# Performance work log

Measured on AMD Instinct MI355X. Metric: run time of the kernel, lower is better.

The kernel has to match this reference:

```python
import jax, jax.numpy as jnp
import numpy as np

N_ELEC = 8192   # electrons (nodes)
N_NUC = 512     # nuclei
EMB = 256       # embedding_dim
KER = 256       # kernel_dim
DF = 64         # dist_feat_dim
MID = 128       # round(sqrt(DF*KER)), log-interpolated hidden width of w-MLP
E = 131072      # edges per edge type


def _ssp(x):
    # shifted softplus, deepqmc default activation: log(0.5*exp(x) + 0.5)
    return jax.nn.softplus(x) - jnp.log(2.0)


def setup_inputs() -> dict:
    key = jax.random.key(0)
    ks = jax.random.split(key, 24)
    def nrm(k, shape, scale):
        return jax.random.normal(k, shape, dtype=jnp.float32) * scale
    inp = {}
    inp['electrons'] = nrm(ks[0], (N_ELEC, EMB), 1.0)
    inp['nuclei'] = nrm(ks[1], (N_NUC, KER), 1.0)
    for i, lbl in enumerate(['same', 'anti', 'n']):
        inp[f'dist_{lbl}'] = jax.random.uniform(ks[2 + i], (E, DF), dtype=jnp.float32)
        inp[f'w1_{lbl}'] = nrm(ks[5 + i], (DF, MID), DF ** -0.5)
        inp[f'b1_{lbl}'] = jnp.zeros((MID,), jnp.float32)
        inp[f'w2_{lbl}'] = nrm(ks[8 + i], (MID, KER), MID ** -0.5)
        inp[f'g_{lbl}'] = nrm(ks[11 + i], (KER, EMB), KER ** -0.5)
    inp['h_w'] = nrm(ks[14], (EMB, KER), EMB ** -0.5)
    inp['senders_same'] = jax.random.randint(ks[15], (E,), 0, N_ELEC)
    inp['senders_anti'] = jax.random.randint(ks[16], (E,), 0, N_ELEC)
    inp['senders_n'] = jax.random.randint(ks[17], (E,), 0, N_NUC)
    inp['receivers_same'] = jax.random.randint(ks[18], (E,), 0, N_ELEC)
    inp['receivers_anti'] = jax.random.randint(ks[19], (E,), 0, N_ELEC)
    inp['receivers_n'] = jax.random.randint(ks[20], (E,), 0, N_ELEC)
    return inp


def reference(electrons, nuclei, dist_same, dist_anti, dist_n,
              w1_same, b1_same, w2_same, w1_anti, b1_anti, w2_anti,
              w1_n, b1_n, w2_n, g_same, g_anti, g_n, h_w,
              senders_same, senders_anti, senders_n,
              receivers_same, receivers_anti, receivers_n):
    def w_mlp(d, w1, b1, w2):
        # MLP with ('log', 2) hidden layers: linear+bias -> SSP -> last linear (no bias)
        return _ssp(d @ w1 + b1) @ w2

    # per-edge filters from distance features: [E, KER]
    we_same = w_mlp(dist_same, w1_same, b1_same, w2_same)
    we_anti = w_mlp(dist_anti, w1_anti, b1_anti, w2_anti)
    we_n = w_mlp(dist_n, w1_n, b1_n, w2_n)

    # shared h (single bias-free linear) on gathered sender electrons: [E, KER]
    hx_same = electrons[senders_same] @ h_w
    hx_anti = electrons[senders_anti] @ h_w

    weh_same = we_same * hx_same
    weh_anti = we_anti * hx_anti
    weh_n = we_n * nuclei[senders_n]

    # scatter-sum messages to receiver electrons: [N_ELEC, KER]
    z_same = jax.ops.segment_sum(weh_same, receivers_same, num_segments=N_ELEC)
    z_anti = jax.ops.segment_sum(weh_anti, receivers_anti, num_segments=N_ELEC)
    z_n = jax.ops.segment_sum(weh_n, receivers_n, num_segments=N_ELEC)

    # per-label g (single bias-free linear) + residual update, order matches original
    return electrons + (z_n @ g_n + z_same @ g_same + z_anti @ g_anti)
```

## Files before the change

kernel.cpp:

```cpp
#include <hip/hip_runtime.h>
#include <stdint.h>


#define N_ELEC 8192
#define N_NUC  512
#define EMB    256
#define KER    256
#define DF     64
#define MID    128
#define NEDGE  131072
#define RPS    8256
#define CSTR   272
#define ASTR_HE 528
#define ASTR_FN 1552

using u16 = unsigned short;
using u64 = unsigned long long;
typedef short short8 __attribute__((ext_vector_type(8)));
typedef float f32x4 __attribute__((ext_vector_type(4)));

__device__ __forceinline__ float bf2f(u16 h) {
  return __uint_as_float(((unsigned)h) << 16);
}
__device__ __forceinline__ u16 f2bf(float f) {
  unsigned u = __float_as_uint(f);
  return (u16)((u + 0x7FFFu + ((u >> 16) & 1u)) >> 16);
}
__device__ __forceinline__ unsigned pkbf(float a, float b) {
  return ((unsigned)f2bf(b) << 16) | (unsigned)f2bf(a);
}
__device__ __forceinline__ float ssp_fast(float x) {
  const float e = __expf(-fabsf(x));
  return fmaxf(x, 0.f) + __logf(fmaf(0.5f, e, 0.5f));
}

__device__ __forceinline__ void bar_lds() {
  __builtin_amdgcn_sched_barrier(0);
  asm volatile("s_waitcnt lgkmcnt(0)" ::: "memory");
  __builtin_amdgcn_s_barrier();
  __builtin_amdgcn_sched_barrier(0);
}

__global__ __launch_bounds__(256) void k_setup(
    const float* h_w, const float* w1s, const float* w1a, const float* w1n,
    const float* w2s, const float* w2a, const float* w2n, const float* gs,
    const float* ga, const float* gn, const int* r0, const int* r1,
    const int* r2, u16* hwT, u16* w1T, u16* w2T, u16* gT, float4* z,
    int* cnt) {
  const int b = blockIdx.x;
  if (b < 6144) {
    z[b * 256 + threadIdx.x] = (float4){0.f, 0.f, 0.f, 0.f};
    return;
  }
  if (b >= 7648) {
    const int eb = b - 7648;
    const int t = eb >> 9;
    const int* rcv = t == 0 ? r0 : (t == 1 ? r1 : r2);
    const int e = ((eb & 511) << 8) + threadIdx.x;
    atomicAdd(&cnt[t * N_ELEC + rcv[e]], 1);
    return;
  }
  int i = (b - 6144) * 256 + threadIdx.x;
  if (i < 65536) {
    int n = i >> 8, k = i & 255;
    hwT[i] = f2bf(h_w[k * 256 + n]);
    return;
  }
  int j = i - 65536;
  if (j < 24576) {
    int t = j >> 13, jj = j & 8191, n = jj >> 6, k = jj & 63;
    const float* w1 = t == 0 ? w1s : (t == 1 ? w1a : w1n);
    w1T[j] = f2bf(w1[k * 128 + n]);
    return;
  }
  j -= 24576;
  if (j < 98304) {
    int t = j >> 15, jj = j & 32767, n = jj >> 7, k = jj & 127;
    const float* w2 = t == 0 ? w2s : (t == 1 ? w2a : w2n);
    w2T[j] = f2bf(w2[k * 256 + n]);
    return;
  }
  j -= 98304;
  if (j < 196608) {
    int n = j / 768, q = j % 768, t = q >> 8, k = q & 255;
    const float* g = t == 0 ? gs : (t == 1 ? ga : gn);
    gT[j] = f2bf(g[k * 256 + n]);
  }
}

__global__ __launch_bounds__(256) void k_scan(const int* cnt, int* rowptr,
                                              int* cursor) {
  const int t = blockIdx.x, tid = threadIdx.x;
  __shared__ int part[256];
  const int* c = cnt + t * N_ELEC;
  int s = 0;
#pragma unroll
  for (int i = 0; i < 32; ++i) s += c[tid * 32 + i];
  part[tid] = s;
  __syncthreads();
  for (int off = 1; off < 256; off <<= 1) {
    int v = (tid >= off) ? part[tid - off] : 0;
    __syncthreads();
    part[tid] += v;
    __syncthreads();
  }
  int run = (tid == 0) ? 0 : part[tid - 1];
  int* rp = rowptr + t * RPS;
  int* cu = cursor + t * N_ELEC;
  for (int i = 0; i < 32; ++i) {
    rp[tid * 32 + i] = run;
    cu[tid * 32 + i] = run;
    run += c[tid * 32 + i];
  }
  if (tid == 255) rp[N_ELEC] = run;
}

__global__ __launch_bounds__(256) void k_place_he(
    const int* r0, const int* r1, const int* r2, const int* s0, const int* s1,
    const int* s2, int* cursor, u64* pk, const float* elec, const u16* hwT,
    u16* he) {
  __shared__ __align__(16) char As[32 * ASTR_HE];
  const int bid = blockIdx.x, tid = threadIdx.x;
  if (bid < 1536) {
    const int t = bid >> 9;
    const int* rcv = t == 0 ? r0 : (t == 1 ? r1 : r2);
    const int* snd = t == 0 ? s0 : (t == 1 ? s1 : s2);
    const int e = ((bid & 511) << 8) + tid;
    const int rr = rcv[e];
    const int pos = atomicAdd(&cursor[t * N_ELEC + rr], 1);
    pk[t * NEDGE + pos] = (u64)(unsigned)e | ((u64)(unsigned)snd[e] << 17) |
                          ((u64)(unsigned)rr << 30);
    return;
  }
  const int m0 = (bid - 1536) * 32;
#pragma unroll
  for (int i = 0; i < 16; ++i) {
    const int idx = i * 256 + tid;
    const int row = idx >> 7, cp = idx & 127;
    const float2 v = *(const float2*)(elec + (long)(m0 + row) * 256 + cp * 2);
    *(unsigned*)(As + row * ASTR_HE + cp * 4) = pkbf(v.x, v.y);
  }
  __syncthreads();
  const int l = tid & 63, lane15 = l & 15, quad = l >> 4, wv = tid >> 6;
  const int nw = wv * 64;
  f32x4 acc[2][4];
#pragma unroll
  for (int i = 0; i < 2; ++i)
#pragma unroll
    for (int j = 0; j < 4; ++j) acc[i][j] = (f32x4){0.f, 0.f, 0.f, 0.f};
  for (int kt = 0; kt < 256; kt += 32) {
    short8 af[2], bf[4];
#pragma unroll
    for (int i = 0; i < 2; ++i)
      af[i] = *(const short8*)(As + (i * 16 + lane15) * ASTR_HE + kt * 2 +
                               quad * 16);
#pragma unroll
    for (int i = 0; i < 4; ++i)
      bf[i] = *(const short8*)(hwT + (nw + i * 16 + lane15) * 256 + kt +
                               quad * 8);
#pragma unroll
    for (int mi = 0; mi < 2; ++mi)
#pragma unroll
      for (int ni = 0; ni < 4; ++ni)
        acc[mi][ni] = __builtin_amdgcn_mfma_f32_16x16x32_bf16(
            af[mi], bf[ni], acc[mi][ni], 0, 0, 0);
  }
#pragma unroll
  for (int mi = 0; mi < 2; ++mi)
#pragma unroll
    for (int r = 0; r < 4; ++r) {
      const int row = m0 + mi * 16 + quad * 4 + r;
#pragma unroll
      for (int ni = 0; ni < 4; ++ni) {
        const int col = nw + ni * 16 + lane15;
        he[row * 256 + col] = f2bf(acc[mi][ni][r]);
      }
    }
}

__global__ __launch_bounds__(256, 3) void k_edge(
    const float* d0, const float* d1, const float* d2, const float* b0,
    const float* b1p, const float* b2, const u16* w1T, const u16* w2T,
    const u16* he, const float* nucf, const u64* pk, float* z) {
  __shared__ char mid[128 * CSTR];
  __shared__ char hc[64 * CSTR];
  __shared__ int snd_l[128], rcv_l[128];

  const int t = blockIdx.z;
  const int m0 = blockIdx.x * 128;
  const int tid = threadIdx.x;
  const float* dist = t == 0 ? d0 : (t == 1 ? d1 : d2);
  const float* bias = t == 0 ? b0 : (t == 1 ? b1p : b2);
  const u16* w1t = w1T + t * 8192;
  const u16* w2t = w2T + t * 32768;
  const bool is_nuc = (t == 2);
  const u64* pkt = pk + (size_t)t * NEDGE + m0;

  if (tid < 128) {
    const u64 rec = pkt[tid];
    snd_l[tid] = (int)((rec >> 17) & 0x1FFFu);
    rcv_l[tid] = (int)(rec >> 30);
  }

  int rows[4];
#pragma unroll
  for (int s = 0; s < 4; ++s)
    rows[s] = (int)(pkt[(s * 256 + tid) >> 3] & 0x1FFFFu);
#pragma unroll
  for (int j = 0; j < 2; ++j)
#pragma unroll
    for (int s = 0; s < 4; ++s) {
      const int idx = s * 256 + tid, row = idx >> 3, ch = idx & 7;
      const float4 v =
          *(const float4*)(dist + (long)rows[s] * 64 + j * 32 + ch * 4);
      uint2 p;
      p.x = pkbf(v.x, v.y);
      p.y = pkbf(v.z, v.w);
      *(uint2*)(mid + j * 8192 + row * 64 + ch * 8) = p;
    }
  bar_lds();

  const int l = tid & 63, lane15 = l & 15, quad = l >> 4, wv = tid >> 6;
  const int mw = (wv >> 1) * 64, nw = (wv & 1) * 64;

  f32x4 acc[4][4];
#pragma unroll
  for (int i = 0; i < 4; ++i)
#pragma unroll
    for (int j = 0; j < 4; ++j) acc[i][j] = (f32x4){0.f, 0.f, 0.f, 0.f};
#pragma unroll
  for (int j = 0; j < 2; ++j) {
    short8 af[4], bf[4];
#pragma unroll
    for (int i = 0; i < 4; ++i) {
      af[i] = *(const short8*)(mid + j * 8192 + (mw + i * 16 + lane15) * 64 +
                               quad * 16);
      bf[i] = *(const short8*)(w1t + (nw + i * 16 + lane15) * 64 + j * 32 +
                               quad * 8);
    }
    __builtin_amdgcn_s_setprio(1);
#pragma unroll
    for (int mi = 0; mi < 4; ++mi)
#pragma unroll
      for (int ni = 0; ni < 4; ++ni)
        acc[mi][ni] = __builtin_amdgcn_mfma_f32_16x16x32_bf16(
            af[mi], bf[ni], acc[mi][ni], 0, 0, 0);
    __builtin_amdgcn_s_setprio(0);
  }
  bar_lds();

#pragma unroll
  for (int mi = 0; mi < 4; ++mi)
#pragma unroll
    for (int r = 0; r < 4; ++r) {
      const int row = mw + mi * 16 + quad * 4 + r;
#pragma unroll
      for (int ni = 0; ni < 4; ++ni) {
        const int col = nw + ni * 16 + lane15;
        const float x = acc[mi][ni][r] + bias[col];
        *(u16*)(mid + row * CSTR + col * 2) = f2bf(ssp_fast(x));
      }
    }
  bar_lds();

  for (int n0 = 0; n0 < 256; n0 += 128) {
#pragma unroll
    for (int i = 0; i < 4; ++i)
#pragma unroll
      for (int j = 0; j < 4; ++j) acc[i][j] = (f32x4){0.f, 0.f, 0.f, 0.f};
#pragma unroll
    for (int kt = 0; kt < 128; kt += 32) {
      short8 af[4], bf[4];
#pragma unroll
      for (int i = 0; i < 4; ++i) {
        af[i] = *(const short8*)(mid + (mw + i * 16 + lane15) * CSTR + kt * 2 +
                                 quad * 16);
        bf[i] = *(const short8*)(w2t + (n0 + nw + i * 16 + lane15) * 128 + kt +
                                 quad * 8);
      }
      __builtin_amdgcn_s_setprio(1);
#pragma unroll
      for (int mi = 0; mi < 4; ++mi)
#pragma unroll
        for (int ni = 0; ni < 4; ++ni)
          acc[mi][ni] = __builtin_amdgcn_mfma_f32_16x16x32_bf16(
              af[mi], bf[ni], acc[mi][ni], 0, 0, 0);
      __builtin_amdgcn_s_setprio(0);
    }

    for (int h = 0; h < 2; ++h) {
      const int rbase = h * 64;
      if (!is_nuc) {
#pragma unroll
        for (int c = 0; c < 4; ++c) {
          const int chunk = c * 256 + tid;
          const int row = chunk >> 4, off = chunk & 15;
          const uint4 v =
              *(const uint4*)((const char*)he +
                              (size_t)snd_l[rbase + row] * 512 + n0 * 2 +
                              off * 16);
          *(uint4*)(hc + row * CSTR + off * 16) = v;
        }
      } else {
#pragma unroll
        for (int c = 0; c < 4; ++c) {
          const int chunk = c * 256 + tid;
          const int row = chunk >> 4, off = chunk & 15;
          const char* src = (const char*)nucf +
                            (size_t)snd_l[rbase + row] * 1024 + n0 * 4 +
                            off * 32;
          const float4 a = *(const float4*)src;
          const float4 b = *(const float4*)(src + 16);
          uint4 p;
          p.x = pkbf(a.x, a.y);
          p.y = pkbf(a.z, a.w);
          p.z = pkbf(b.x, b.y);
          p.w = pkbf(b.z, b.w);
          *(uint4*)(hc + row * CSTR + off * 16) = p;
        }
      }
      bar_lds();

      if ((wv >> 1) == h) {
#pragma unroll
        for (int mi = 0; mi < 4; ++mi)
#pragma unroll
          for (int r = 0; r < 4; ++r) {
            const int lrow = mi * 16 + quad * 4 + r;
#pragma unroll
            for (int ni = 0; ni < 4; ++ni) {
              const int col = nw + ni * 16 + lane15;
              u16* p = (u16*)(hc + lrow * CSTR) + col;
              *p = f2bf(acc[mi][ni][r] * bf2f(*p));
            }
          }
      }
      bar_lds();

      {
        const int cp = l;
        const int rbeg = wv * 16, rend = rbeg + 16;
        float a0 = 0.f, a1 = 0.f;
        int cur = rcv_l[rbase + rbeg];
        for (int row = rbeg; row < rend; ++row) {
          const unsigned p = *(const unsigned*)(hc + row * CSTR + cp * 4);
          a0 += __uint_as_float(p << 16);
          a1 += __uint_as_float(p & 0xffff0000u);
          const int nxt = (row + 1 < rend) ? rcv_l[rbase + row + 1] : -1;
          if (nxt != cur) {
            float* zp = z + (size_t)cur * 768 + t * 256 + n0 + cp * 2;
            unsafeAtomicAdd(zp, a0);
            unsafeAtomicAdd(zp + 1, a1);
            a0 = a1 = 0.f;
            cur = nxt;
          }
        }
      }
      bar_lds();
    }
  }
}

__global__ __launch_bounds__(256) void k_final(const float* z, const u16* gT,
                                               const float* elec, float* out) {
  __shared__ __align__(16) char As[32 * ASTR_FN];
  const int tid = threadIdx.x;
  const int m0 = blockIdx.x * 32;
#pragma unroll
  for (int i = 0; i < 24; ++i) {
    const int idx = i * 256 + tid;
    const int row = idx / 192, q = idx % 192;
    const float4 v = *(const float4*)(z + (long)(m0 + row) * 768 + q * 4);
    uint2 p;
    p.x = pkbf(v.x, v.y);
    p.y = pkbf(v.z, v.w);
    *(uint2*)(As + row * ASTR_FN + q * 8) = p;
  }
  __syncthreads();
  const int l = tid & 63, lane15 = l & 15, quad = l >> 4, wv = tid >> 6;
  const int nw = wv * 64;
  f32x4 acc[2][4];
#pragma unroll
  for (int i = 0; i < 2; ++i)
#pragma unroll
    for (int j = 0; j < 4; ++j) acc[i][j] = (f32x4){0.f, 0.f, 0.f, 0.f};
  for (int kt = 0; kt < 768; kt += 32) {
    short8 af[2], bf[4];
#pragma unroll
    for (int i = 0; i < 2; ++i)
      af[i] = *(const short8*)(As + (i * 16 + lane15) * ASTR_FN + kt * 2 +
                               quad * 16);
#pragma unroll
    for (int i = 0; i < 4; ++i)
      bf[i] = *(const short8*)(gT + (nw + i * 16 + lane15) * 768 + kt +
                               quad * 8);
#pragma unroll
    for (int mi = 0; mi < 2; ++mi)
#pragma unroll
      for (int ni = 0; ni < 4; ++ni)
        acc[mi][ni] = __builtin_amdgcn_mfma_f32_16x16x32_bf16(
            af[mi], bf[ni], acc[mi][ni], 0, 0, 0);
  }
#pragma unroll
  for (int mi = 0; mi < 2; ++mi)
#pragma unroll
    for (int r = 0; r < 4; ++r) {
      const int row = m0 + mi * 16 + quad * 4 + r;
#pragma unroll
      for (int ni = 0; ni < 4; ++ni) {
        const int col = nw + ni * 16 + lane15;
        out[row * 256 + col] = acc[mi][ni][r] + elec[row * 256 + col];
      }
    }
}

extern "C" void kernel_launch(void* const* d_in, const int* in_sizes, int n_in,
                              void* d_out, int out_size, void* d_ws,
                              size_t ws_size, hipStream_t stream) {
  int I_dist[3], I_w1[3], I_b1[3], I_w2[3], I_g[3], I_hw;
  if (in_sizes[3] == 64 * 128) {
    for (int t = 0; t < 3; ++t) {
      I_dist[t] = 2 + t * 5 + 0;
      I_w1[t] = 2 + t * 5 + 1;
      I_b1[t] = 2 + t * 5 + 2;
      I_w2[t] = 2 + t * 5 + 3;
      I_g[t] = 2 + t * 5 + 4;
    }
    I_hw = 17;
  } else {
    I_dist[0] = 2; I_dist[1] = 3; I_dist[2] = 4;
    I_w1[0] = 5;  I_b1[0] = 6;  I_w2[0] = 7;
    I_w1[1] = 8;  I_b1[1] = 9;  I_w2[1] = 10;
    I_w1[2] = 11; I_b1[2] = 12; I_w2[2] = 13;
    I_g[0] = 14; I_g[1] = 15; I_g[2] = 16;
    I_hw = 17;
  }
  const int I_snd[3] = {18, 19, 20};
  const int I_rcv[3] = {21, 22, 23};

  char* ws = (char*)d_ws;
  u16* he = (u16*)(ws + 0);
  u16* hwT = (u16*)(ws + 4194304);
  u16* w1T = (u16*)(ws + 4325376);
  u16* w2T = (u16*)(ws + 4374528);
  u16* gT = (u16*)(ws + 4571136);
  float* z = (float*)(ws + 4964352);
  int* cnt = (int*)(ws + 30130176);
  int* rowptr = (int*)(ws + 30228480);
  int* cursor = (int*)(ws + 30327552);
  u64* pk = (u64*)(ws + 30425856);

  const float* elec = (const float*)d_in[0];
  const float* nuc = (const float*)d_in[1];
  const int* s0 = (const int*)d_in[I_snd[0]];
  const int* s1 = (const int*)d_in[I_snd[1]];
  const int* s2 = (const int*)d_in[I_snd[2]];
  const int* r0 = (const int*)d_in[I_rcv[0]];
  const int* r1 = (const int*)d_in[I_rcv[1]];
  const int* r2 = (const int*)d_in[I_rcv[2]];

  hipMemsetAsync(cnt, 0, 98304, stream);

  k_setup<<<9184, 256, 0, stream>>>(
      (const float*)d_in[I_hw], (const float*)d_in[I_w1[0]],
      (const float*)d_in[I_w1[1]], (const float*)d_in[I_w1[2]],
      (const float*)d_in[I_w2[0]], (const float*)d_in[I_w2[1]],
      (const float*)d_in[I_w2[2]], (const float*)d_in[I_g[0]],
      (const float*)d_in[I_g[1]], (const float*)d_in[I_g[2]], r0, r1, r2,
      hwT, w1T, w2T, gT, (float4*)z, cnt);

  k_scan<<<3, 256, 0, stream>>>(cnt, rowptr, cursor);

  k_place_he<<<1792, 256, 0, stream>>>(r0, r1, r2, s0, s1, s2, cursor, pk,
                                       elec, hwT, he);

  k_edge<<<dim3(NEDGE / 128, 1, 3), 256, 0, stream>>>(
      (const float*)d_in[I_dist[0]], (const float*)d_in[I_dist[1]],
      (const float*)d_in[I_dist[2]], (const float*)d_in[I_b1[0]],
      (const float*)d_in[I_b1[1]], (const float*)d_in[I_b1[2]], w1T, w2T, he,
      nuc, pk, z);

  k_final<<<N_ELEC / 32, 256, 0, stream>>>(z, gT, elec, (float*)d_out);
}
```

Measured before the change: 391.6 us.

## Make edge kernel persistent with prefetch of next tile's indices and distances

The edge kernel now launches 256 blocks per edge type, and each block loops over 4 tiles of 128 edges with a stride of 256 tiles. While the first MLP layer of the current tile runs, it prefetches the next tile's packed sender/receiver records and its distance features into registers, hiding the gather latency behind MFMA work. The risk is higher register pressure from holding eight float4 prefetch buffers, which could reduce occupancy below the 3 blocks per CU target. It also cuts the grid from 3072 to 768 blocks, which may leave some CUs underused or unevenly loaded.

Result: slower. 475.9 us (+21.5%).

```diff
diff --git a/kernel.cpp b/kernel.cpp
--- a/kernel.cpp
+++ b/kernel.cpp
@@ -187,95 +187,78 @@
   __shared__ int snd_l[128], rcv_l[128];
 
   const int t = blockIdx.z;
-  const int m0 = blockIdx.x * 128;
   const int tid = threadIdx.x;
   const float* dist = t == 0 ? d0 : (t == 1 ? d1 : d2);
   const float* bias = t == 0 ? b0 : (t == 1 ? b1p : b2);
   const u16* w1t = w1T + t * 8192;
   const u16* w2t = w2T + t * 32768;
   const bool is_nuc = (t == 2);
-  const u64* pkt = pk + (size_t)t * NEDGE + m0;
-
-  if (tid < 128) {
-    const u64 rec = pkt[tid];
-    snd_l[tid] = (int)((rec >> 17) & 0x1FFFu);
-    rcv_l[tid] = (int)(rec >> 30);
-  }
-
-  int rows[4];
-#pragma unroll
-  for (int s = 0; s < 4; ++s)
-    rows[s] = (int)(pkt[(s * 256 + tid) >> 3] & 0x1FFFFu);
-#pragma unroll
-  for (int j = 0; j < 2; ++j)
-#pragma unroll
-    for (int s = 0; s < 4; ++s) {
-      const int idx = s * 256 + tid, row = idx >> 3, ch = idx & 7;
-      const float4 v =
-          *(const float4*)(dist + (long)rows[s] * 64 + j * 32 + ch * 4);
-      uint2 p;
-      p.x = pkbf(v.x, v.y);
-      p.y = pkbf(v.z, v.w);
-      *(uint2*)(mid + j * 8192 + row * 64 + ch * 8) = p;
-    }
-  bar_lds();
+  const u64* pkbase = pk + (size_t)t * NEDGE;
 
   const int l = tid & 63, lane15 = l & 15, quad = l >> 4, wv = tid >> 6;
   const int mw = (wv >> 1) * 64, nw = (wv & 1) * 64;
 
-  f32x4 acc[4][4];
-#pragma unroll
-  for (int i = 0; i < 4; ++i)
-#pragma unroll
-    for (int j = 0; j < 4; ++j) acc[i][j] = (f32x4){0.f, 0.f, 0.f, 0.f};
-#pragma unroll
-  for (int j = 0; j < 2; ++j) {
-    short8 af[4], bf[4];
-#pragma unroll
-    for (int i = 0; i < 4; ++i) {
-      af[i] = *(const short8*)(mid + j * 8192 + (mw + i * 16 + lane15) * 64 +
-                               quad * 16);
-      bf[i] = *(const short8*)(w1t + (nw + i * 16 + lane15) * 64 + j * 32 +
-                               quad * 8);
-    }
-    __builtin_amdgcn_s_setprio(1);
-#pragma unroll
-    for (int mi = 0; mi < 4; ++mi)
-#pragma unroll
-      for (int ni = 0; ni < 4; ++ni)
-        acc[mi][ni] = __builtin_amdgcn_mfma_f32_16x16x32_bf16(
-            af[mi], bf[ni], acc[mi][ni], 0, 0, 0);
-    __builtin_amdgcn_s_setprio(0);
-  }
-  bar_lds();
-
-#pragma unroll
-  for (int mi = 0; mi < 4; ++mi)
-#pragma unroll
-    for (int r = 0; r < 4; ++r) {
-      const int row = mw + mi * 16 + quad * 4 + r;
-#pragma unroll
-      for (int ni = 0; ni < 4; ++ni) {
-        const int col = nw + ni * 16 + lane15;
-        const float x = acc[mi][ni][r] + bias[col];
-        *(u16*)(mid + row * CSTR + col * 2) = f2bf(ssp_fast(x));
-      }
-    }
-  bar_lds();
-
-  for (int n0 = 0; n0 < 256; n0 += 128) {
+  int tile = blockIdx.x;
+  u64 rec_pf = 0;
+  int rows_pf[4];
+  float4 dv[2][4];
+  {
+    const u64* pkt = pkbase + (size_t)tile * 128;
+    if (tid < 128) rec_pf = pkt[tid];
+#pragma unroll
+    for (int s = 0; s < 4; ++s)
+      rows_pf[s] = (int)(pkt[(s * 256 + tid) >> 3] & 0x1FFFFu);
+#pragma unroll
+    for (int j = 0; j < 2; ++j)
+#pragma unroll
+      for (int s = 0; s < 4; ++s) {
+        const int ch = (s * 256 + tid) & 7;
+        dv[j][s] =
+            *(const float4*)(dist + (long)rows_pf[s] * 64 + j * 32 + ch * 4);
+      }
+  }
+
+  for (int it = 0; it < 4; ++it) {
+    if (tid < 128) {
+      snd_l[tid] = (int)((rec_pf >> 17) & 0x1FFFu);
+      rcv_l[tid] = (int)(rec_pf >> 30);
+    }
+#pragma unroll
+    for (int j = 0; j < 2; ++j)
+#pragma unroll
+      for (int s = 0; s < 4; ++s) {
+        const int idx = s * 256 + tid, row = idx >> 3, ch = idx & 7;
+        uint2 p;
+        p.x = pkbf(dv[j][s].x, dv[j][s].y);
+        p.y = pkbf(dv[j][s].z, dv[j][s].w);
+        *(uint2*)(mid + j * 8192 + row * 64 + ch * 8) = p;
+      }
+    bar_lds();
+
+    u64 rec_n = 0;
+    int rows_n[4];
+    const int ntile = tile + 256;
+    if (it < 3) {
+      const u64* pn = pkbase + (size_t)ntile * 128;
+      if (tid < 128) rec_n = pn[tid];
+#pragma unroll
+      for (int s = 0; s < 4; ++s)
+        rows_n[s] = (int)(pn[(s * 256 + tid) >> 3] & 0x1FFFFu);
+    }
+
+    f32x4 acc[4][4];
 #pragma unroll
     for (int i = 0; i < 4; ++i)
 #pragma unroll
       for (int j = 0; j < 4; ++j) acc[i][j] = (f32x4){0.f, 0.f, 0.f, 0.f};
 #pragma unroll
-    for (int kt = 0; kt < 128; kt += 32) {
+    for (int j = 0; j < 2; ++j) {
       short8 af[4], bf[4];
 #pragma unroll
       for (int i = 0; i < 4; ++i) {
-        af[i] = *(const short8*)(mid + (mw + i * 16 + lane15) * CSTR + kt * 2 +
+        af[i] = *(const short8*)(mid + j * 8192 + (mw + i * 16 + lane15) * 64 +
                                  quad * 16);
-        bf[i] = *(const short8*)(w2t + (n0 + nw + i * 16 + lane15) * 128 + kt +
+        bf[i] = *(const short8*)(w1t + (nw + i * 16 + lane15) * 64 + j * 32 +
                                  quad * 8);
       }
       __builtin_amdgcn_s_setprio(1);
@@ -287,77 +270,131 @@
               af[mi], bf[ni], acc[mi][ni], 0, 0, 0);
       __builtin_amdgcn_s_setprio(0);
     }
-
-    for (int h = 0; h < 2; ++h) {
-      const int rbase = h * 64;
-      if (!is_nuc) {
-#pragma unroll
-        for (int c = 0; c < 4; ++c) {
-          const int chunk = c * 256 + tid;
-          const int row = chunk >> 4, off = chunk & 15;
-          const uint4 v =
-              *(const uint4*)((const char*)he +
-                              (size_t)snd_l[rbase + row] * 512 + n0 * 2 +
-                              off * 16);
-          *(uint4*)(hc + row * CSTR + off * 16) = v;
+    bar_lds();
+
+    if (it < 3) {
+#pragma unroll
+      for (int j = 0; j < 2; ++j)
+#pragma unroll
+        for (int s = 0; s < 4; ++s) {
+          const int ch = (s * 256 + tid) & 7;
+          dv[j][s] =
+              *(const float4*)(dist + (long)rows_n[s] * 64 + j * 32 + ch * 4);
         }
-      } else {
-#pragma unroll
-        for (int c = 0; c < 4; ++c) {
-          const int chunk = c * 256 + tid;
-          const int row = chunk >> 4, off = chunk & 15;
-          const char* src = (const char*)nucf +
-                            (size_t)snd_l[rbase + row] * 1024 + n0 * 4 +
-                            off * 32;
-          const float4 a = *(const float4*)src;
-          const float4 b = *(const float4*)(src + 16);
-          uint4 p;
-          p.x = pkbf(a.x, a.y);
-          p.y = pkbf(a.z, a.w);
-          p.z = pkbf(b.x, b.y);
-          p.w = pkbf(b.z, b.w);
-          *(uint4*)(hc + row * CSTR + off * 16) = p;
+    }
+
+#pragma unroll
+    for (int mi = 0; mi < 4; ++mi)
+#pragma unroll
+      for (int r = 0; r < 4; ++r) {
+        const int row = mw + mi * 16 + quad * 4 + r;
+#pragma unroll
+        for (int ni = 0; ni < 4; ++ni) {
+          const int col = nw + ni * 16 + lane15;
+          const float x = acc[mi][ni][r] + bias[col];
+          *(u16*)(mid + row * CSTR + col * 2) = f2bf(ssp_fast(x));
         }
       }
-      bar_lds();
-
-      if ((wv >> 1) == h) {
+    bar_lds();
+
+    for (int n0 = 0; n0 < 256; n0 += 128) {
+#pragma unroll
+      for (int i = 0; i < 4; ++i)
+#pragma unroll
+        for (int j = 0; j < 4; ++j) acc[i][j] = (f32x4){0.f, 0.f, 0.f, 0.f};
+#pragma unroll
+      for (int kt = 0; kt < 128; kt += 32) {
+        short8 af[4], bf[4];
+#pragma unroll
+        for (int i = 0; i < 4; ++i) {
+          af[i] = *(const short8*)(mid + (mw + i * 16 + lane15) * CSTR +
+                                   kt * 2 + quad * 16);
+          bf[i] = *(const short8*)(w2t + (n0 + nw + i * 16 + lane15) * 128 +
+                                   kt + quad * 8);
+        }
+        __builtin_amdgcn_s_setprio(1);
 #pragma unroll
         for (int mi = 0; mi < 4; ++mi)
 #pragma unroll
-          for (int r = 0; r < 4; ++r) {
-            const int lrow = mi * 16 + quad * 4 + r;
-#pragma unroll
-            for (int ni = 0; ni < 4; ++ni) {
-              const int col = nw + ni * 16 + lane15;
-              u16* p = (u16*)(hc + lrow * CSTR) + col;
-              *p = f2bf(acc[mi][ni][r] * bf2f(*p));
+          for (int ni = 0; ni < 4; ++ni)
+            acc[mi][ni] = __builtin_amdgcn_mfma_f32_16x16x32_bf16(
+                af[mi], bf[ni], acc[mi][ni], 0, 0, 0);
+        __builtin_amdgcn_s_setprio(0);
+      }
+
+      for (int h = 0; h < 2; ++h) {
+        const int rbase = h * 64;
+        if (!is_nuc) {
+#pragma unroll
+          for (int c = 0; c < 4; ++c) {
+            const int chunk = c * 256 + tid;
+            const int row = chunk >> 4, off = chunk & 15;
+            const uint4 v =
+                *(const uint4*)((const char*)he +
+                                (size_t)snd_l[rbase + row] * 512 + n0 * 2 +
+                                off * 16);
+            *(uint4*)(hc + row * CSTR + off * 16) = v;
+          }
+        } else {
+#pragma unroll
+          for (int c = 0; c < 4; ++c) {
+            const int chunk = c * 256 + tid;
+            const int row = chunk >> 4, off = chunk & 15;
+            const char* src = (const char*)nucf +
+                              (size_t)snd_l[rbase + row] * 1024 + n0 * 4 +
+                              off * 32;
+            const float4 a = *(const float4*)src;
+            const float4 b = *(const float4*)(src + 16);
+            uint4 p;
+            p.x = pkbf(a.x, a.y);
+            p.y = pkbf(a.z, a.w);
+            p.z = pkbf(b.x, b.y);
+            p.w = pkbf(b.z, b.w);
+            *(uint4*)(hc + row * CSTR + off * 16) = p;
+          }
+        }
+        bar_lds();
+
+        if ((wv >> 1) == h) {
+#pragma unroll
+          for (int mi = 0; mi < 4; ++mi)
+#pragma unroll
+            for (int r = 0; r < 4; ++r) {
+              const int lrow = mi * 16 + quad * 4 + r;
+#pragma unroll
+              for (int ni = 0; ni < 4; ++ni) {
+                const int col = nw + ni * 16 + lane15;
+                u16* p = (u16*)(hc + lrow * CSTR) + col;
+                *p = f2bf(acc[mi][ni][r] * bf2f(*p));
+              }
+            }
+        }
+        bar_lds();
+
+        {
+          const int cp = l;
+          const int rbeg = wv * 16, rend = rbeg + 16;
+          float a0 = 0.f, a1 = 0.f;
+          int cur = rcv_l[rbase + rbeg];
+          for (int row = rbeg; row < rend; ++row) {
+            const unsigned p = *(const unsigned*)(hc + row * CSTR + cp * 4);
+            a0 += __uint_as_float(p << 16);
+            a1 += __uint_as_float(p & 0xffff0000u);
+            const int nxt = (row + 1 < rend) ? rcv_l[rbase + row + 1] : -1;
+            if (nxt != cur) {
+              float* zp = z + (size_t)cur * 768 + t * 256 + n0 + cp * 2;
+              unsafeAtomicAdd(zp, a0);
+              unsafeAtomicAdd(zp + 1, a1);
+              a0 = a1 = 0.f;
+              cur = nxt;
             }
           }
-      }
-      bar_lds();
-
-      {
-        const int cp = l;
-        const int rbeg = wv * 16, rend = rbeg + 16;
-        float a0 = 0.f, a1 = 0.f;
-        int cur = rcv_l[rbase + rbeg];
-        for (int row = rbeg; row < rend; ++row) {
-          const unsigned p = *(const unsigned*)(hc + row * CSTR + cp * 4);
-          a0 += __uint_as_float(p << 16);
-          a1 += __uint_as_float(p & 0xffff0000u);
-          const int nxt = (row + 1 < rend) ? rcv_l[rbase + row + 1] : -1;
-          if (nxt != cur) {
-            float* zp = z + (size_t)cur * 768 + t * 256 + n0 + cp * 2;
-            unsafeAtomicAdd(zp, a0);
-            unsafeAtomicAdd(zp + 1, a1);
-            a0 = a1 = 0.f;
-            cur = nxt;
-          }
         }
-      }
-      bar_lds();
-    }
+        bar_lds();
+      }
+    }
+    rec_pf = rec_n;
+    tile = ntile;
   }
 }
 
@@ -474,7 +511,7 @@
   k_place_he<<<1792, 256, 0, stream>>>(r0, r1, r2, s0, s1, s2, cursor, pk,
                                        elec, hwT, he);
 
-  k_edge<<<dim3(NEDGE / 128, 1, 3), 256, 0, stream>>>(
+  k_edge<<<dim3(256, 1, 3), 256, 0, stream>>>(
       (const float*)d_in[I_dist[0]], (const float*)d_in[I_dist[1]],
       (const float*)d_in[I_dist[2]], (const float*)d_in[I_b1[0]],
       (const float*)d_in[I_b1[1]], (const float*)d_in[I_b1[2]], w1T, w2T, he,
```
